# Kernel optimization log

Hardware: AMD Instinct MI355X
Metric: run time of the kernel (lower is better)

## Reference

```python
import jax, jax.numpy as jnp
import numpy as np

NUM_ITERATIONS = 3

def squash(t, axis=-1):
    sq = jnp.sum(t * t, axis=axis, keepdims=True)
    scale = sq / (1.0 + sq)
    return scale * t / jnp.sqrt(sq)

def setup_inputs() -> dict:
    key = jax.random.key(0)
    k1, k2 = jax.random.split(key)
    B, N, Ci = 16, 1024, 64
    C, O = 32, 32
    x = jax.random.normal(k1, (B, N, Ci), dtype=jnp.float32)
    route_weights = jax.random.normal(k2, (C, N, Ci, O), dtype=jnp.float32)
    return {"x": x, "route_weights": route_weights}

def reference(x, route_weights):
    # priors: (C, B, N, O)  == torch's (C,B,N,1,O) with singleton squeezed
    priors = jnp.einsum('bni,cnio->cbno', x, route_weights)
    C, B, N, O = priors.shape
    logits = jnp.zeros((C, B, N, 1), dtype=priors.dtype)
    outputs = None
    for i in range(NUM_ITERATIONS):
        probs = jax.nn.softmax(logits, axis=2)  # over route nodes
        outputs = squash(jnp.sum(probs * priors, axis=2, keepdims=True))  # (C,B,1,O)
        if i != NUM_ITERATIONS - 1:
            delta = jnp.sum(priors * outputs, axis=-1, keepdims=True)  # (C,B,N,1)
            logits = logits + delta
    # match torch output shape (C, B, 1, 1, O)
    return outputs[:, :, :, None, :]
```

## Files before the change

kernel.cpp:

```cpp
#include <hip/hip_runtime.h>

constexpr int kB  = 16;
constexpr int kN  = 1024;
constexpr int kCI = 64;
constexpr int kC  = 32;
constexpr int kO  = 32;
constexpr int kNT = 4;

__global__ __launch_bounds__(128) void priors_kernel(
    const float* __restrict__ x,
    const float* rw,
    float* priors, int nstride) {
  const int c  = blockIdx.x >> 8;
  const int n0 = (blockIdx.x & 255) * kNT;
  const int t  = threadIdx.x;

  __shared__ float ws[kNT * kCI * kO];
  __shared__ float xs[kNT * kCI * kB];

  {
    const float4* src = (const float4*)(rw + (size_t)(c * kN + n0) * (kCI * kO));
    float4* dst4 = (float4*)ws;
    #pragma unroll
    for (int it = 0; it < 16; ++it) {
      int f = t + 128 * it;
      dst4[f] = src[f];
    }
  }
  {
    #pragma unroll
    for (int it = 0; it < 8; ++it) {
      int f = t + 128 * it;
      int b = f & 15;
      int a = (f >> 4) & 15;
      int j = f >> 8;
      float4 v = *(const float4*)(x + (size_t)(b * kN + n0 + j) * kCI + a * 4);
      int idx = (j * kCI + a * 4) * kB + b;
      xs[idx +  0] = v.x;
      xs[idx + 16] = v.y;
      xs[idx + 32] = v.z;
      xs[idx + 48] = v.w;
    }
  }
  __syncthreads();

  const int j  = t >> 5;
  const int og = (t & 31) >> 2;
  const int bg = t & 3;
  const float* wp = ws + j * (kCI * kO) + og * 4;
  const float* xp = xs + j * (kCI * kB) + bg * 4;

  float acc[4][4];
  #pragma unroll
  for (int bb = 0; bb < 4; ++bb)
    #pragma unroll
    for (int oo = 0; oo < 4; ++oo) acc[bb][oo] = 0.f;

  #pragma unroll
  for (int i0 = 0; i0 < kCI; i0 += 4) {
    float4 wv[4], xv[4];
    #pragma unroll
    for (int q = 0; q < 4; ++q) wv[q] = *(const float4*)(wp + (i0 + q) * kO);
    #pragma unroll
    for (int q = 0; q < 4; ++q) xv[q] = *(const float4*)(xp + (i0 + q) * kB);
    #pragma unroll
    for (int q = 0; q < 4; ++q) {
      const float* xq = (const float*)&xv[q];
      const float* wq = (const float*)&wv[q];
      #pragma unroll
      for (int bb = 0; bb < 4; ++bb)
        #pragma unroll
        for (int oo = 0; oo < 4; ++oo)
          acc[bb][oo] += xq[bb] * wq[oo];
    }
  }

  float* dst = priors + (size_t)(c * kN + n0) * nstride;
  #pragma unroll
  for (int bb = 0; bb < 4; ++bb) {
    int b = bg * 4 + bb;
    float4 v = make_float4(acc[bb][0], acc[bb][1], acc[bb][2], acc[bb][3]);
    *(float4*)(dst + (size_t)j * nstride + b * kO + og * 4) = v;
  }
}

__global__ __launch_bounds__(256) void routing_kernel(
    const float* priors, int nstride,
    float* __restrict__ out) {
  const int cb = blockIdx.x;
  const int c = cb >> 4, b = cb & 15;
  const int t = threadIdx.x;

  __shared__ float R[256 * 33];
  __shared__ float S2[8 * 33];
  __shared__ float out_lds[kO];
  __shared__ float wred[8];

  const float* base = priors + (size_t)c * kN * nstride + b * kO;

  float p[4][kO];
  #pragma unroll
  for (int k = 0; k < 4; ++k) {
    const float* rp = base + (size_t)(t + 256 * k) * nstride;
    #pragma unroll
    for (int q = 0; q < 8; ++q) {
      float4 v = *(const float4*)(rp + q * 4);
      p[k][q * 4 + 0] = v.x; p[k][q * 4 + 1] = v.y;
      p[k][q * 4 + 2] = v.z; p[k][q * 4 + 3] = v.w;
    }
  }

  float l[4] = {0.f, 0.f, 0.f, 0.f};

  for (int iter = 0; iter < 3; ++iter) {
    if (iter > 0) {
      #pragma unroll
      for (int k = 0; k < 4; ++k) {
        float d = 0.f;
        #pragma unroll
        for (int o = 0; o < kO; ++o) d += p[k][o] * out_lds[o];
        l[k] += d;
      }
    }
    float lm = fmaxf(fmaxf(l[0], l[1]), fmaxf(l[2], l[3]));
    #pragma unroll
    for (int s = 32; s >= 1; s >>= 1) lm = fmaxf(lm, __shfl_xor(lm, s));
    if ((t & 63) == 0) wred[t >> 6] = lm;
    __syncthreads();
    const float m = fmaxf(fmaxf(wred[0], wred[1]), fmaxf(wred[2], wred[3]));

    float acc[kO];
    #pragma unroll
    for (int o = 0; o < kO; ++o) acc[o] = 0.f;
    float denp = 0.f;
    #pragma unroll
    for (int k = 0; k < 4; ++k) {
      float e = __expf(l[k] - m);
      denp += e;
      #pragma unroll
      for (int o = 0; o < kO; ++o) acc[o] += e * p[k][o];
    }
    #pragma unroll
    for (int s = 32; s >= 1; s >>= 1) denp += __shfl_xor(denp, s);
    if ((t & 63) == 0) wred[4 + (t >> 6)] = denp;

    #pragma unroll
    for (int o = 0; o < kO; ++o) R[t * 33 + o] = acc[o];
    __syncthreads();
    {
      int o = t & 31, g = t >> 5;
      float s = 0.f;
      #pragma unroll
      for (int jj = 0; jj < 32; ++jj) s += R[(g * 32 + jj) * 33 + o];
      S2[g * 33 + o] = s;
    }
    __syncthreads();
    if (t < kO) {
      float s = 0.f;
      #pragma unroll
      for (int g = 0; g < 8; ++g) s += S2[g * 33 + t];
      const float den = wred[4] + wred[5] + wred[6] + wred[7];
      s /= den;
      float sq = s * s;
      #pragma unroll
      for (int sh = 16; sh >= 1; sh >>= 1) sq += __shfl_xor(sq, sh);
      const float r = sqrtf(sq);
      const float ov = s * (r / (1.f + sq));
      out_lds[t] = ov;
      if (iter == 2) out[cb * kO + t] = ov;
    }
    __syncthreads();
  }
}

extern "C" void kernel_launch(void* const* d_in, const int* in_sizes, int n_in,
                              void* d_out, int out_size, void* d_ws, size_t ws_size,
                              hipStream_t stream) {
  const float* x  = (const float*)d_in[0];
  const float* rw = (const float*)d_in[1];
  float* out = (float*)d_out;

  const size_t need = (size_t)kC * kN * kB * kO * sizeof(float);
  float* priors;
  int nstride;
  if (ws_size >= need) {
    priors  = (float*)d_ws;
    nstride = kB * kO;
  } else {
    priors  = (float*)const_cast<float*>(rw);
    nstride = kCI * kO;
  }

  priors_kernel<<<dim3(kC * (kN / kNT)), dim3(128), 0, stream>>>(x, rw, priors, nstride);
  routing_kernel<<<dim3(kC * kB), dim3(256), 0, stream>>>(priors, nstride, out);
}
```

Baseline: 395.4 us.

## Stream route weights from global in priors kernel and widen per-thread batch tile

The priors kernel no longer stages the full per-node weight slab in shared memory. Each thread now streams its own float4 weight row directly from global memory and computes all 16 batch entries times 4 outputs for one route node. Only x is staged in shared memory, in 16-channel chunks with a padded stride, and a block covers 32 nodes with 256 threads. The goal is to cut LDS traffic and the staging barrier around the large weight tensor. In exchange, each thread holds 64 accumulators, which raises register pressure, and the weight loads are strided across nodes.

```diff
diff --git a/kernel.cpp b/kernel.cpp
--- a/kernel.cpp
+++ b/kernel.cpp
@@ -5,82 +5,73 @@
 constexpr int kCI = 64;
 constexpr int kC  = 32;
 constexpr int kO  = 32;
-constexpr int kNT = 4;
+constexpr int kNT = 32;
+constexpr int kIC = 16;
+constexpr int XSS = 260;
 
-__global__ __launch_bounds__(128) void priors_kernel(
+
+__global__ __launch_bounds__(256, 4) void priors_kernel(
     const float* __restrict__ x,
     const float* rw,
     float* priors, int nstride) {
-  const int c  = blockIdx.x >> 8;
-  const int n0 = (blockIdx.x & 255) * kNT;
+  const int c  = blockIdx.x >> 5;
+  const int n0 = (blockIdx.x & 31) * kNT;
   const int t  = threadIdx.x;
+  const int og = t & 7;
+  const int nl = t >> 3;
 
-  __shared__ float ws[kNT * kCI * kO];
-  __shared__ float xs[kNT * kCI * kB];
+  __shared__ float xs[kNT * XSS];
 
-  {
-    const float4* src = (const float4*)(rw + (size_t)(c * kN + n0) * (kCI * kO));
-    float4* dst4 = (float4*)ws;
+  float acc[kB][4];
+  #pragma unroll
+  for (int b = 0; b < kB; ++b)
     #pragma unroll
-    for (int it = 0; it < 16; ++it) {
-      int f = t + 128 * it;
-      dst4[f] = src[f];
-    }
-  }
-  {
+    for (int o = 0; o < 4; ++o) acc[b][o] = 0.f;
+
+  const float* rwp = rw + (size_t)(c * kN + n0 + nl) * (kCI * kO) + og * 4;
+
+  for (int ch = 0; ch < kCI / kIC; ++ch) {
+    const int i0 = ch * kIC;
+    if (ch) __syncthreads();
     #pragma unroll
     for (int it = 0; it < 8; ++it) {
-      int f = t + 128 * it;
-      int b = f & 15;
-      int a = (f >> 4) & 15;
-      int j = f >> 8;
-      float4 v = *(const float4*)(x + (size_t)(b * kN + n0 + j) * kCI + a * 4);
-      int idx = (j * kCI + a * 4) * kB + b;
-      xs[idx +  0] = v.x;
-      xs[idx + 16] = v.y;
-      xs[idx + 32] = v.z;
-      xs[idx + 48] = v.w;
+      int f  = it * 256 + t;
+      int ii = f & 3;
+      int nn = (f >> 2) & 31;
+      int b  = f >> 7;
+      float4 v = *(const float4*)(x + (size_t)(b * kN + n0 + nn) * kCI + i0 + ii * 4);
+      float* d = xs + nn * XSS + (ii * 4) * kB + b;
+      d[0]  = v.x;
+      d[16] = v.y;
+      d[32] = v.z;
+      d[48] = v.w;
     }
-  }
-  __syncthreads();
-
-  const int j  = t >> 5;
-  const int og = (t & 31) >> 2;
-  const int bg = t & 3;
-  const float* wp = ws + j * (kCI * kO) + og * 4;
-  const float* xp = xs + j * (kCI * kB) + bg * 4;
-
-  float acc[4][4];
-  #pragma unroll
-  for (int bb = 0; bb < 4; ++bb)
+    __syncthreads();
     #pragma unroll
-    for (int oo = 0; oo < 4; ++oo) acc[bb][oo] = 0.f;
-
-  #pragma unroll
-  for (int i0 = 0; i0 < kCI; i0 += 4) {
-    float4 wv[4], xv[4];
-    #pragma unroll
-    for (int q = 0; q < 4; ++q) wv[q] = *(const float4*)(wp + (i0 + q) * kO);
-    #pragma unroll
-    for (int q = 0; q < 4; ++q) xv[q] = *(const float4*)(xp + (i0 + q) * kB);
-    #pragma unroll
-    for (int q = 0; q < 4; ++q) {
-      const float* xq = (const float*)&xv[q];
-      const float* wq = (const float*)&wv[q];
+    for (int il = 0; il < kIC; ++il) {
+      const int i = i0 + il;
+      float4 w = *(const float4*)(rwp + (size_t)i * kO);
+      const float* xp = xs + nl * XSS + il * kB;
+      float4 xb[4];
       #pragma unroll
-      for (int bb = 0; bb < 4; ++bb)
-        #pragma unroll
-        for (int oo = 0; oo < 4; ++oo)
-          acc[bb][oo] += xq[bb] * wq[oo];
+      for (int q = 0; q < 4; ++q) xb[q] = *(const float4*)(xp + q * 4);
+      const float* xf = (const float*)xb;
+      #pragma unroll
+      for (int b = 0; b < kB; ++b) {
+        const float xv = xf[b];
+        acc[b][0] += xv * w.x;
+        acc[b][1] += xv * w.y;
+        acc[b][2] += xv * w.z;
+        acc[b][3] += xv * w.w;
+      }
     }
   }
 
-  float* dst = priors + (size_t)(c * kN + n0) * nstride;
+  float* dst = priors + (size_t)(c * kN + n0 + nl) * nstride + og * 4;
   #pragma unroll
-  for (int bb = 0; bb < 4; ++bb) {
-    int b = bg * 4 + bb;
-    float4 v = make_float4(acc[bb][0], acc[bb][1], acc[bb][2], acc[bb][3]);
-    *(float4*)(dst + (size_t)j * nstride + b * kO + og * 4) = v;
+  for (int b = 0; b < kB; ++b) {
+    float4 v = make_float4(acc[b][0], acc[b][1], acc[b][2], acc[b][3]);
+    *(float4*)(dst + (size_t)b * kO) = v;
   }
 }
 
@@ -191,6 +182,6 @@
     nstride = kCI * kO;
   }
 
-  priors_kernel<<<dim3(kC * (kN / kNT)), dim3(128), 0, stream>>>(x, rw, priors, nstride);
+  priors_kernel<<<dim3(kC * (kN / kNT)), dim3(256), 0, stream>>>(x, rw, priors, nstride);
   routing_kernel<<<dim3(kC * kB), dim3(256), 0, stream>>>(priors, nstride, out);
 }
```

New measurement: 419.6 us. +6.1%, slower.
